# Kernel tuning notes

Measured on AMD Instinct MI355X. Metric: run time of the kernel, lower is better.

The kernel has to match this reference:

```python
import jax, jax.numpy as jnp
import numpy as np

SOS_TOKEN = 1
MAX_LENGTH = 64
VOCAB = 32000
HIDDEN = 1024
BATCH = 32


def setup_inputs() -> dict:
    key = jax.random.key(0)
    ks = jax.random.split(key, 10)
    s = 1.0 / np.sqrt(HIDDEN)
    return {
        "encoder_outputs": jax.random.normal(ks[0], (BATCH, MAX_LENGTH, HIDDEN), dtype=jnp.float32),
        "encoder_hidden": jax.random.normal(ks[1], (1, BATCH, HIDDEN), dtype=jnp.float32),
        "target_tensor": jax.random.randint(ks[2], (BATCH, MAX_LENGTH), 0, VOCAB),
        "embedding": jax.random.normal(ks[3], (VOCAB, HIDDEN), dtype=jnp.float32),
        "W_ih": jax.random.uniform(ks[4], (3 * HIDDEN, HIDDEN), jnp.float32, -s, s),
        "W_hh": jax.random.uniform(ks[5], (3 * HIDDEN, HIDDEN), jnp.float32, -s, s),
        "b_ih": jax.random.uniform(ks[6], (3 * HIDDEN,), jnp.float32, -s, s),
        "b_hh": jax.random.uniform(ks[7], (3 * HIDDEN,), jnp.float32, -s, s),
        "out_W": jax.random.uniform(ks[8], (VOCAB, HIDDEN), jnp.float32, -s, s),
        "out_b": jax.random.uniform(ks[9], (VOCAB,), jnp.float32, -s, s),
    }


def _decode(encoder_hidden, target_tensor, embedding, W_ih, W_hh, b_ih, b_hh, out_W, out_b):
    B = target_tensor.shape[0]
    # teacher forcing: input at step i is SOS (i=0) else target[:, i-1]
    sos = jnp.full((B, 1), SOS_TOKEN, dtype=target_tensor.dtype)
    inputs = jnp.concatenate([sos, target_tensor[:, :-1]], axis=1)  # [B,T]
    x = jax.nn.relu(embedding[inputs])  # [B,T,H]
    # precompute all input-side gate projections in one GEMM: [B,T,3H]
    xg = jnp.einsum("bth,gh->btg", x, W_ih) + b_ih
    h0 = encoder_hidden[0]  # [B,H]

    def step(h, xg_t):
        hg = h @ W_hh.T + b_hh  # [B,3H]
        xr, xz, xn = jnp.split(xg_t, 3, axis=-1)
        hr, hz, hn = jnp.split(hg, 3, axis=-1)
        r = jax.nn.sigmoid(xr + hr)
        z = jax.nn.sigmoid(xz + hz)
        n = jnp.tanh(xn + r * hn)
        h_new = (1.0 - z) * n + z * h
        return h_new, h_new

    h_last, hs = jax.lax.scan(step, h0, jnp.swapaxes(xg, 0, 1))
    hs = jnp.swapaxes(hs, 0, 1)  # [B,T,H]
    logits = jnp.einsum("bth,vh->btv", hs, out_W) + out_b
    log_probs = jax.nn.log_softmax(logits, axis=-1)
    return log_probs, h_last[None]  # hidden shaped [1,B,H] like torch GRU


def reference(encoder_outputs, encoder_hidden, target_tensor, embedding, W_ih, W_hh, b_ih, b_hh, out_W, out_b):
    del encoder_outputs  # only used for batch size in the original
    return _decode(encoder_hidden, target_tensor, embedding, W_ih, W_hh, b_ih, b_hh, out_W, out_b)
```

## Files before the change

### kernel.cpp

```cpp
#include <hip/hip_runtime.h>
#include <hip/hip_bf16.h>

#define B_ 32
#define T_ 64
#define H_ 1024
#define G3 3072
#define V_ 32000
#define M_ 2048
#define NB_SCAN 64
#define NTILE_N 250

typedef __attribute__((ext_vector_type(8))) short s16x8;
typedef __attribute__((ext_vector_type(4))) float f32x4;
typedef __bf16 bf16x8 __attribute__((ext_vector_type(8)));

__device__ inline unsigned short f2bf(float f) {
    union { float f; unsigned int u; } v; v.f = f;
    unsigned int u = v.u;
    return (unsigned short)((u + 0x7FFFu + ((u >> 16) & 1u)) >> 16);
}

__device__ inline s16x8 load_b128_cc(const void* p) {
    s16x8 r;
    asm volatile("global_load_dwordx4 %0, %1, off sc0 sc1" : "=v"(r) : "v"(p));
    return r;
}
__device__ inline unsigned int load_b32_cc(const void* p) {
    unsigned int r;
    asm volatile("global_load_dword %0, %1, off sc0 sc1" : "=v"(r) : "v"(p));
    return r;
}
__device__ inline void store_b32_cc(void* p, unsigned int v) {
    asm volatile("global_store_dword %0, %1, off sc0 sc1" :: "v"(p), "v"(v) : "memory");
}

__global__ __launch_bounds__(256) void prep_all(
    const float* __restrict__ W_ih, const float* __restrict__ W_hh,
    const float* __restrict__ out_W,
    unsigned short* __restrict__ wihb, unsigned short* __restrict__ whhb,
    unsigned short* __restrict__ owb,
    const int* __restrict__ target, const float* __restrict__ emb,
    unsigned short* __restrict__ xb,
    const float* __restrict__ enc_hidden, unsigned short* __restrict__ hb0,
    unsigned int* __restrict__ flg)
{
    int gid = blockIdx.x * 256 + threadIdx.x;
    int gs = gridDim.x * 256;
    const int NW = G3 * H_ / 4;
    const int NO = V_ * H_ / 4;

    for (int i = gid; i < NW; i += gs) {
        float4 v = *(const float4*)(W_ih + (size_t)i * 4);
        ushort4 o; o.x = f2bf(v.x); o.y = f2bf(v.y); o.z = f2bf(v.z); o.w = f2bf(v.w);
        *(ushort4*)(wihb + (size_t)i * 4) = o;
    }
    for (int i = gid; i < NW; i += gs) {
        float4 v = *(const float4*)(W_hh + (size_t)i * 4);
        ushort4 o; o.x = f2bf(v.x); o.y = f2bf(v.y); o.z = f2bf(v.z); o.w = f2bf(v.w);
        *(ushort4*)(whhb + (size_t)i * 4) = o;
    }
    for (int i = gid; i < NO; i += gs) {
        float4 v = *(const float4*)(out_W + (size_t)i * 4);
        ushort4 o; o.x = f2bf(v.x); o.y = f2bf(v.y); o.z = f2bf(v.z); o.w = f2bf(v.w);
        *(ushort4*)(owb + (size_t)i * 4) = o;
    }
    for (int i = gid; i < M_ * 256; i += gs) {
        int m = i >> 8, k = (i & 255) * 4;
        int b = m >> 6, t = m & 63;
        int tok = (t == 0) ? 1 : target[b * T_ + t - 1];
        float4 v = *(const float4*)(emb + (size_t)tok * H_ + k);
        ushort4 o;
        o.x = f2bf(fmaxf(v.x, 0.f)); o.y = f2bf(fmaxf(v.y, 0.f));
        o.z = f2bf(fmaxf(v.z, 0.f)); o.w = f2bf(fmaxf(v.w, 0.f));
        *(ushort4*)(xb + (size_t)m * H_ + k) = o;
    }
    for (int i = gid; i < B_ * H_; i += gs) hb0[i] = f2bf(enc_hidden[i]);
    for (int i = gid; i < 128; i += gs) flg[i] = 0;
}

__global__ __launch_bounds__(256) void gemm_bias(
    const unsigned short* __restrict__ A,
    const unsigned short* __restrict__ Bm,
    const float* __restrict__ bias,
    float* __restrict__ C,
    int N, int K)
{
    __shared__ __align__(16) unsigned short As[2 * 4096];
    __shared__ __align__(16) unsigned short Bs[2 * 4096];
    int n0 = blockIdx.x * 128, m0 = blockIdx.y * 128;
    int tid = threadIdx.x;
    int lane = tid & 63, wv = tid >> 6;
    int wr = wv >> 1, wc = wv & 1;

    f32x4 acc[4][4] = {};

    int o0 = wv * 2048 + lane * 16;
    int row0 = o0 >> 6, ib0 = (o0 & 63) >> 1;
    int o1 = o0 + 1024;
    int row1 = o1 >> 6, ib1 = (o1 & 63) >> 1;

    auto stage = [&](int buf, int k0) {
        const unsigned short* ga0 = A + (size_t)(m0 + row0) * K + k0 + ib0;
        const unsigned short* gb0 = Bm + (size_t)(n0 + row0) * K + k0 + ib0;
        const unsigned short* ga1 = A + (size_t)(m0 + row1) * K + k0 + ib1;
        const unsigned short* gb1 = Bm + (size_t)(n0 + row1) * K + k0 + ib1;
        unsigned short* la0 = As + buf * 4096 + wv * 1024;
        unsigned short* lb0 = Bs + buf * 4096 + wv * 1024;
        __builtin_amdgcn_global_load_lds((const __attribute__((address_space(1))) void*)ga0,
                                         (__attribute__((address_space(3))) void*)la0, 16, 0, 0);
        __builtin_amdgcn_global_load_lds((const __attribute__((address_space(1))) void*)gb0,
                                         (__attribute__((address_space(3))) void*)lb0, 16, 0, 0);
        __builtin_amdgcn_global_load_lds((const __attribute__((address_space(1))) void*)ga1,
                                         (__attribute__((address_space(3))) void*)(la0 + 512), 16, 0, 0);
        __builtin_amdgcn_global_load_lds((const __attribute__((address_space(1))) void*)gb1,
                                         (__attribute__((address_space(3))) void*)(lb0 + 512), 16, 0, 0);
    };

    int kq = (lane >> 4) * 8;
    int rA = wr * 64 + (lane & 15);
    int rB = wc * 64 + (lane & 15);

    int NT = K >> 5;
    stage(0, 0);
    __syncthreads();

    int cur = 0;
    for (int t = 0; t < NT; ++t) {
        if (t + 1 < NT) stage(cur ^ 1, (t + 1) << 5);
        const unsigned short* ab = As + cur * 4096;
        const unsigned short* bb = Bs + cur * 4096;
        s16x8 af[4], bf[4];
#pragma unroll
        for (int i = 0; i < 4; ++i) {
            af[i] = *(const s16x8*)(ab + (rA + i * 16) * 32 + kq);
            bf[i] = *(const s16x8*)(bb + (rB + i * 16) * 32 + kq);
        }
#pragma unroll
        for (int mf = 0; mf < 4; ++mf)
#pragma unroll
            for (int nf = 0; nf < 4; ++nf)
                acc[mf][nf] = __builtin_amdgcn_mfma_f32_16x16x32_bf16(
                    __builtin_bit_cast(bf16x8, af[mf]),
                    __builtin_bit_cast(bf16x8, bf[nf]),
                    acc[mf][nf], 0, 0, 0);
        __syncthreads();
        cur ^= 1;
    }

#pragma unroll
    for (int nf = 0; nf < 4; ++nf) {
        int col = n0 + wc * 64 + nf * 16 + (lane & 15);
        float bv = bias[col];
#pragma unroll
        for (int mf = 0; mf < 4; ++mf) {
            int mbase = m0 + wr * 64 + mf * 16 + (lane >> 4) * 4;
#pragma unroll
            for (int r = 0; r < 4; ++r)
                C[(size_t)(mbase + r) * N + col] = acc[mf][nf][r] + bv;
        }
    }
}

__global__ __launch_bounds__(256) void gemm_logits(
    const unsigned short* __restrict__ A,
    const unsigned short* __restrict__ Bm,
    const float* __restrict__ bias,
    float* __restrict__ C,
    float* __restrict__ pmax,
    float* __restrict__ psum)
{
    __shared__ __align__(16) unsigned short As[2 * 4096];
    __shared__ __align__(16) unsigned short Bs[2 * 4096];
    __shared__ float spx[2][128], sps[2][128];
    int m0 = blockIdx.x * 128;
    int ntile = blockIdx.y;
    int n0 = ntile * 128;
    int tid = threadIdx.x;
    int lane = tid & 63, wv = tid >> 6;
    int wr = wv >> 1, wc = wv & 1;

    f32x4 acc[4][4] = {};

    int o0 = wv * 2048 + lane * 16;
    int row0 = o0 >> 6, ib0 = (o0 & 63) >> 1;
    int o1 = o0 + 1024;
    int row1 = o1 >> 6, ib1 = (o1 & 63) >> 1;

    auto stage = [&](int buf, int k0) {
        const unsigned short* ga0 = A + (size_t)(m0 + row0) * H_ + k0 + ib0;
        const unsigned short* gb0 = Bm + (size_t)(n0 + row0) * H_ + k0 + ib0;
        const unsigned short* ga1 = A + (size_t)(m0 + row1) * H_ + k0 + ib1;
        const unsigned short* gb1 = Bm + (size_t)(n0 + row1) * H_ + k0 + ib1;
        unsigned short* la0 = As + buf * 4096 + wv * 1024;
        unsigned short* lb0 = Bs + buf * 4096 + wv * 1024;
        __builtin_amdgcn_global_load_lds((const __attribute__((address_space(1))) void*)ga0,
                                         (__attribute__((address_space(3))) void*)la0, 16, 0, 0);
        __builtin_amdgcn_global_load_lds((const __attribute__((address_space(1))) void*)gb0,
                                         (__attribute__((address_space(3))) void*)lb0, 16, 0, 0);
        __builtin_amdgcn_global_load_lds((const __attribute__((address_space(1))) void*)ga1,
                                         (__attribute__((address_space(3))) void*)(la0 + 512), 16, 0, 0);
        __builtin_amdgcn_global_load_lds((const __attribute__((address_space(1))) void*)gb1,
                                         (__attribute__((address_space(3))) void*)(lb0 + 512), 16, 0, 0);
    };

    int q = lane >> 4, rr2 = lane & 15;
    int kq = q * 8;
    int rA = wr * 64 + rr2;
    int rB = wc * 64 + rr2;

    stage(0, 0);
    __syncthreads();

    int cur = 0;
    for (int t = 0; t < 32; ++t) {
        if (t + 1 < 32) stage(cur ^ 1, (t + 1) << 5);
        const unsigned short* ab = As + cur * 4096;
        const unsigned short* bb = Bs + cur * 4096;
        s16x8 af[4], bf[4];
#pragma unroll
        for (int i = 0; i < 4; ++i) {
            af[i] = *(const s16x8*)(ab + (rA + i * 16) * 32 + kq);
            bf[i] = *(const s16x8*)(bb + (rB + i * 16) * 32 + kq);
        }
#pragma unroll
        for (int mf = 0; mf < 4; ++mf)
#pragma unroll
            for (int nf = 0; nf < 4; ++nf)
                acc[mf][nf] = __builtin_amdgcn_mfma_f32_16x16x32_bf16(
                    __builtin_bit_cast(bf16x8, af[mf]),
                    __builtin_bit_cast(bf16x8, bf[nf]),
                    acc[mf][nf], 0, 0, 0);
        __syncthreads();
        cur ^= 1;
    }

    float bv[4];
#pragma unroll
    for (int nf = 0; nf < 4; ++nf) bv[nf] = bias[n0 + wc * 64 + nf * 16 + rr2];

#pragma unroll
    for (int mf = 0; mf < 4; ++mf) {
#pragma unroll
        for (int r = 0; r < 4; ++r) {
            int row_local = wr * 64 + mf * 16 + q * 4 + r;
            float vmax = -1e30f;
#pragma unroll
            for (int nf = 0; nf < 4; ++nf) vmax = fmaxf(vmax, acc[mf][nf][r] + bv[nf]);
#pragma unroll
            for (int o = 1; o < 16; o <<= 1) vmax = fmaxf(vmax, __shfl_xor(vmax, o));
            float vsum = 0.f;
#pragma unroll
            for (int nf = 0; nf < 4; ++nf) vsum += __expf(acc[mf][nf][r] + bv[nf] - vmax);
#pragma unroll
            for (int o = 1; o < 16; o <<= 1) vsum += __shfl_xor(vsum, o);
            if (rr2 == 0) { spx[wc][row_local] = vmax; sps[wc][row_local] = vsum; }
        }
    }

#pragma unroll
    for (int nf = 0; nf < 4; ++nf) {
        int col = n0 + wc * 64 + nf * 16 + rr2;
#pragma unroll
        for (int mf = 0; mf < 4; ++mf) {
            int mbase = m0 + wr * 64 + mf * 16 + q * 4;
#pragma unroll
            for (int r = 0; r < 4; ++r)
                C[(size_t)(mbase + r) * V_ + col] = acc[mf][nf][r] + bv[nf];
        }
    }

    __syncthreads();
    if (wc == 0 && rr2 == 0) {
#pragma unroll
        for (int mf = 0; mf < 4; ++mf)
#pragma unroll
            for (int r = 0; r < 4; ++r) {
                int row_local = wr * 64 + mf * 16 + q * 4 + r;
                float m0v = spx[0][row_local], m1v = spx[1][row_local];
                float Mv = fmaxf(m0v, m1v);
                float Sv = sps[0][row_local] * __expf(m0v - Mv) + sps[1][row_local] * __expf(m1v - Mv);
                pmax[(size_t)(m0 + row_local) * NTILE_N + ntile] = Mv;
                psum[(size_t)(m0 + row_local) * NTILE_N + ntile] = Sv;
            }
    }
}

__global__ __launch_bounds__(256) void gru_scan(
    const unsigned short* __restrict__ Whhb,
    const float* __restrict__ b_hh,
    const float* __restrict__ enc_hidden,
    const float* __restrict__ xg,
    unsigned short* __restrict__ hb0, unsigned short* __restrict__ hb1,
    float* __restrict__ hfF,
    unsigned short* __restrict__ hs,
    unsigned int* __restrict__ flags)
{
    __shared__ __align__(16) unsigned short ws_[48 * 1024];
    __shared__ __align__(16) f32x4 red[2][3][64];

    int tid = threadIdx.x;
    int lane = tid & 63, wave = tid >> 6;
    int rt = wave >> 1, kh = wave & 1;
    int ct = blockIdx.x;

    for (int idx = tid; idx < 48 * 128; idx += 256) {
        int r = idx >> 7, slot = idx & 127;
        int g = r >> 4, jr = r & 15;
        s16x8 v = *(const s16x8*)(Whhb + (size_t)(g * H_ + ct * 16 + jr) * H_ + slot * 8);
        *(s16x8*)(ws_ + r * 1024 + (slot ^ (r & 7)) * 8) = v;
    }
    __syncthreads();

    int rr = lane & 15, q = lane >> 4;
    int col = ct * 16 + rr;
    int xsw = rr & 7;
    int kbase = kh * 512;
    int sbase = kh * 64 + q;
    float br = b_hh[col], bz = b_hh[H_ + col], bn = b_hh[2 * H_ + col];
    int b0 = rt * 16 + q * 4;

    float hold[4];
    float xr[4], xz[4], xn[4];
    if (kh == 1) {
#pragma unroll
        for (int r = 0; r < 4; ++r) {
            hold[r] = enc_hidden[(b0 + r) * H_ + col];
            const float* xrow = xg + ((size_t)(b0 + r) * T_) * G3;
            xr[r] = xrow[col]; xz[r] = xrow[H_ + col]; xn[r] = xrow[2 * H_ + col];
        }
    }

    for (int t = 0; t < T_; ++t) {
        const unsigned short* hbp = (t & 1) ? hb1 : hb0;
        unsigned short*       hbn = (t & 1) ? hb0 : hb1;

        const unsigned short* ha = hbp + (size_t)(rt * 16 + rr) * H_ + kbase + q * 8;
        s16x8 af[16];
#pragma unroll
        for (int i = 0; i < 16; ++i) af[i] = load_b128_cc(ha + i * 32);

        f32x4 accr, accz, accn;
        if (kh == 1) {
            accr = (f32x4){br, br, br, br};
            accz = (f32x4){bz, bz, bz, bz};
            accn = (f32x4){bn, bn, bn, bn};
        } else {
            accr = (f32x4){0.f, 0.f, 0.f, 0.f};
            accz = accr; accn = accr;
        }

        asm volatile("s_waitcnt vmcnt(0)");
        __builtin_amdgcn_sched_barrier(0);

#pragma unroll
        for (int kk = 0; kk < 16; ++kk) {
            int so = ((sbase + kk * 4) ^ xsw) * 8;
            s16x8 fr = *(const s16x8*)(ws_ + rr * 1024 + so);
            s16x8 fz = *(const s16x8*)(ws_ + (16 + rr) * 1024 + so);
            s16x8 fn = *(const s16x8*)(ws_ + (32 + rr) * 1024 + so);
            bf16x8 a = __builtin_bit_cast(bf16x8, af[kk]);
            accr = __builtin_amdgcn_mfma_f32_16x16x32_bf16(a, __builtin_bit_cast(bf16x8, fr), accr, 0, 0, 0);
            accz = __builtin_amdgcn_mfma_f32_16x16x32_bf16(a, __builtin_bit_cast(bf16x8, fz), accz, 0, 0, 0);
            accn = __builtin_amdgcn_mfma_f32_16x16x32_bf16(a, __builtin_bit_cast(bf16x8, fn), accn, 0, 0, 0);
        }

        if (kh == 0) {
            red[rt][0][lane] = accr; red[rt][1][lane] = accz; red[rt][2][lane] = accn;
        }
        __syncthreads();
        if (kh == 1) {
            accr += red[rt][0][lane]; accz += red[rt][1][lane]; accn += red[rt][2][lane];
            unsigned int hpk[4];
#pragma unroll
            for (int r = 0; r < 4; ++r) {
                float rg = 1.f / (1.f + __expf(-(xr[r] + accr[r])));
                float zg = 1.f / (1.f + __expf(-(xz[r] + accz[r])));
                float ng = tanhf(xn[r] + rg * accn[r]);
                float hnew = (1.f - zg) * ng + zg * hold[r];
                hold[r] = hnew;
                hpk[r] = f2bf(hnew);
            }
#pragma unroll
            for (int r = 0; r < 4; ++r) {
                unsigned int other = __shfl_xor((int)hpk[r], 1);
                if ((rr & 1) == 0) {
                    unsigned int pk = hpk[r] | (other << 16);
                    store_b32_cc(hbn + (size_t)(b0 + r) * H_ + col, pk);
                    *(unsigned int*)(hs + ((size_t)(b0 + r) * T_ + t) * H_ + col) = pk;
                }
            }
            if (t == T_ - 1) {
#pragma unroll
                for (int r = 0; r < 4; ++r) hfF[(b0 + r) * H_ + col] = hold[r];
            }
            asm volatile("s_waitcnt vmcnt(0)" ::: "memory");
        }

        if (t < T_ - 1) {
            __syncthreads();
            if (tid == 0) store_b32_cc(flags + ct, (unsigned int)(t + 1));
            if (kh == 1) {
#pragma unroll
                for (int r = 0; r < 4; ++r) {
                    const float* xrow = xg + ((size_t)(b0 + r) * T_ + (t + 1)) * G3;
                    xr[r] = xrow[col]; xz[r] = xrow[H_ + col]; xn[r] = xrow[2 * H_ + col];
                }
                __builtin_amdgcn_sched_barrier(0);
            }
            unsigned int tgt = (unsigned int)(t + 1);
            while (true) {
                unsigned int f = load_b32_cc(flags + lane);
                asm volatile("s_waitcnt vmcnt(0)");
                if (__all(f >= tgt)) break;
                __builtin_amdgcn_s_sleep(1);
            }
            __builtin_amdgcn_sched_barrier(0);
        }
    }
}

__global__ __launch_bounds__(256) void lse_sub_copy(
    float* __restrict__ out,
    const float* __restrict__ pmax, const float* __restrict__ psum,
    const float* __restrict__ hfF)
{
    int m = blockIdx.x;
    int tid = threadIdx.x;
    __shared__ float sm[4], ssum[4];

    if (m < B_) {
        float4 v = *(const float4*)(hfF + m * H_ + tid * 4);
        *(float4*)(out + (size_t)M_ * V_ + m * H_ + tid * 4) = v;
    }

    float M = -1e30f, S = 0.f;
    for (int i = tid; i < NTILE_N; i += 256) {
        float pm_ = pmax[(size_t)m * NTILE_N + i];
        float ps_ = psum[(size_t)m * NTILE_N + i];
        float nm = fmaxf(M, pm_);
        S = S * __expf(M - nm) + ps_ * __expf(pm_ - nm);
        M = nm;
    }
    for (int o = 32; o > 0; o >>= 1) {
        float om = __shfl_xor(M, o), os = __shfl_xor(S, o);
        float nm = fmaxf(M, om);
        S = S * __expf(M - nm) + os * __expf(om - nm);
        M = nm;
    }
    int wv = tid >> 6, lane = tid & 63;
    if (lane == 0) { sm[wv] = M; ssum[wv] = S; }
    __syncthreads();
    float fm = fmaxf(fmaxf(sm[0], sm[1]), fmaxf(sm[2], sm[3]));
    float fs = ssum[0] * __expf(sm[0] - fm) + ssum[1] * __expf(sm[1] - fm)
             + ssum[2] * __expf(sm[2] - fm) + ssum[3] * __expf(sm[3] - fm);
    float lse = fm + __logf(fs);

    float* row = out + (size_t)m * V_;
    for (int i = tid * 4; i < V_; i += 1024) {
        float4 v = *(const float4*)(row + i);
        v.x -= lse; v.y -= lse; v.z -= lse; v.w -= lse;
        *(float4*)(row + i) = v;
    }
}

extern "C" void kernel_launch(void* const* d_in, const int* in_sizes, int n_in,
                              void* d_out, int out_size, void* d_ws, size_t ws_size,
                              hipStream_t stream) {
    const float* enc_hidden = (const float*)d_in[1];
    const int*   target     = (const int*)d_in[2];
    const float* embedding  = (const float*)d_in[3];
    const float* W_ih       = (const float*)d_in[4];
    const float* W_hh       = (const float*)d_in[5];
    const float* b_ih       = (const float*)d_in[6];
    const float* b_hh       = (const float*)d_in[7];
    const float* out_W      = (const float*)d_in[8];
    const float* out_b      = (const float*)d_in[9];
    float* out = (float*)d_out;

    char* ws = (char*)d_ws;
    float*          xg   = (float*)(ws);
    unsigned short* xb   = (unsigned short*)(ws + 25165824);
    unsigned short* hsb  = (unsigned short*)(ws + 29360128);
    unsigned short* wihb = (unsigned short*)(ws + 33554432);
    unsigned short* whhb = (unsigned short*)(ws + 39845888);
    unsigned short* owb  = (unsigned short*)(ws + 46137344);
    float*          hfF  = (float*)(ws + 111673344);
    unsigned short* hb0  = (unsigned short*)(ws + 111804416);
    unsigned short* hb1  = (unsigned short*)(ws + 111869952);
    unsigned int*   flg  = (unsigned int*)(ws + 111935488);
    float*          pmx  = (float*)(ws + 25165824);
    float*          psm  = (float*)(ws + 25165824 + 2048000);

    prep_all<<<2048, 256, 0, stream>>>(W_ih, W_hh, out_W, wihb, whhb, owb,
                                       target, embedding, xb, enc_hidden, hb0, flg);

    gemm_bias<<<dim3(G3 / 128, M_ / 128), 256, 0, stream>>>(xb, wihb, b_ih, xg, G3, H_);

    {
        void* args[] = { (void*)&whhb, (void*)&b_hh, (void*)&enc_hidden, (void*)&xg,
                         (void*)&hb0, (void*)&hb1, (void*)&hfF, (void*)&hsb, (void*)&flg };
        hipLaunchCooperativeKernel((const void*)gru_scan, dim3(NB_SCAN), dim3(256), args, 0, stream);
    }

    gemm_logits<<<dim3(M_ / 128, NTILE_N), 256, 0, stream>>>(hsb, owb, out_b, out, pmx, psm);

    lse_sub_copy<<<M_, 256, 0, stream>>>(out, pmx, psm, hfF);
}
```

Baseline: 885.8 us.

## Triple-buffer GEMM LDS staging with partial vmcnt waits

Both bf16 GEMM kernels move from double to triple buffering of the LDS A/B tiles, prefetching two K-steps ahead. The full __syncthreads is replaced by explicit s_waitcnt vmcnt(4), which waits only for the older tile's global->LDS loads, followed by a raw s_barrier. The goal is to keep more global loads in flight and hide memory latency behind the MFMA work. In exchange LDS use per block grows from 32KB to 48KB, which may cut occupancy, and correctness now relies on hand-counted vmcnt values.

Measured after the change: 894.9 us. No clear change (+1.0%).

```diff
diff --git a/kernel.cpp b/kernel.cpp
--- a/kernel.cpp
+++ b/kernel.cpp
@@ -85,8 +85,8 @@
     float* __restrict__ C,
     int N, int K)
 {
-    __shared__ __align__(16) unsigned short As[2 * 4096];
-    __shared__ __align__(16) unsigned short Bs[2 * 4096];
+    __shared__ __align__(16) unsigned short As[3 * 4096];
+    __shared__ __align__(16) unsigned short Bs[3 * 4096];
     int n0 = blockIdx.x * 128, m0 = blockIdx.y * 128;
     int tid = threadIdx.x;
     int lane = tid & 63, wv = tid >> 6;
@@ -122,11 +122,21 @@
 
     int NT = K >> 5;
     stage(0, 0);
-    __syncthreads();
+    if (NT > 1) {
+        stage(1, 32);
+        asm volatile("s_waitcnt vmcnt(4)");
+    } else {
+        asm volatile("s_waitcnt vmcnt(0)");
+    }
+    __builtin_amdgcn_s_barrier();
+    __builtin_amdgcn_sched_barrier(0);
 
     int cur = 0;
     for (int t = 0; t < NT; ++t) {
-        if (t + 1 < NT) stage(cur ^ 1, (t + 1) << 5);
+        if (t + 2 < NT) {
+            int nb = cur + 2; if (nb >= 3) nb -= 3;
+            stage(nb, (t + 2) << 5);
+        }
         const unsigned short* ab = As + cur * 4096;
         const unsigned short* bb = Bs + cur * 4096;
         s16x8 af[4], bf[4];
@@ -143,8 +153,14 @@
                     __builtin_bit_cast(bf16x8, af[mf]),
                     __builtin_bit_cast(bf16x8, bf[nf]),
                     acc[mf][nf], 0, 0, 0);
-        __syncthreads();
-        cur ^= 1;
+        if (t + 1 < NT) {
+            if (t + 2 < NT) asm volatile("s_waitcnt vmcnt(4)");
+            else            asm volatile("s_waitcnt vmcnt(0)");
+            asm volatile("s_waitcnt lgkmcnt(0)");
+            __builtin_amdgcn_s_barrier();
+            __builtin_amdgcn_sched_barrier(0);
+        }
+        cur = (cur == 2) ? 0 : cur + 1;
     }
 
 #pragma unroll
@@ -169,8 +185,8 @@
     float* __restrict__ pmax,
     float* __restrict__ psum)
 {
-    __shared__ __align__(16) unsigned short As[2 * 4096];
-    __shared__ __align__(16) unsigned short Bs[2 * 4096];
+    __shared__ __align__(16) unsigned short As[3 * 4096];
+    __shared__ __align__(16) unsigned short Bs[3 * 4096];
     __shared__ float spx[2][128], sps[2][128];
     int m0 = blockIdx.x * 128;
     int ntile = blockIdx.y;
@@ -209,11 +225,17 @@
     int rB = wc * 64 + rr2;
 
     stage(0, 0);
-    __syncthreads();
+    stage(1, 32);
+    asm volatile("s_waitcnt vmcnt(4)");
+    __builtin_amdgcn_s_barrier();
+    __builtin_amdgcn_sched_barrier(0);
 
     int cur = 0;
     for (int t = 0; t < 32; ++t) {
-        if (t + 1 < 32) stage(cur ^ 1, (t + 1) << 5);
+        if (t + 2 < 32) {
+            int nb = cur + 2; if (nb >= 3) nb -= 3;
+            stage(nb, (t + 2) << 5);
+        }
         const unsigned short* ab = As + cur * 4096;
         const unsigned short* bb = Bs + cur * 4096;
         s16x8 af[4], bf[4];
@@ -230,8 +252,14 @@
                     __builtin_bit_cast(bf16x8, af[mf]),
                     __builtin_bit_cast(bf16x8, bf[nf]),
                     acc[mf][nf], 0, 0, 0);
-        __syncthreads();
-        cur ^= 1;
+        if (t + 1 < 32) {
+            if (t + 2 < 32) asm volatile("s_waitcnt vmcnt(4)");
+            else            asm volatile("s_waitcnt vmcnt(0)");
+            asm volatile("s_waitcnt lgkmcnt(0)");
+            __builtin_amdgcn_s_barrier();
+            __builtin_amdgcn_sched_barrier(0);
+        }
+        cur = (cur == 2) ? 0 : cur + 1;
     }
 
     float bv[4];
```
